# Performance work log

Hardware: AMD Instinct MI355X
Metric: run time of the kernel (lower is better)

The kernel has to match this reference:

```python
import jax, jax.numpy as jnp
import numpy as np
import math

VOCAB, SEQ, D_MODEL, H, D_FF, N_LAYERS = 32000, 2048, 768, 12, 3072, 6
D_K = D_MODEL // H
EPS = 1e-7


def _pos_encoding(seq, d):
    pos = jnp.arange(seq, dtype=jnp.float32)[:, None]
    i = jnp.arange(d)[None, :]
    rates = 1.0 / jnp.power(10000.0, (2 * (i // 2)).astype(jnp.float32) / d)
    ang = pos * rates
    return jnp.where(i % 2 == 0, jnp.sin(ang), jnp.cos(ang))  # [seq, d]


def _layernorm(x, alpha, beta):
    # faithful to source: scalar alpha/beta, population std, std+eps in denom
    mean = jnp.mean(x, axis=-1, keepdims=True)
    std = jnp.std(x, axis=-1, keepdims=True)
    return alpha * (x - mean) / (std + EPS) + beta


def setup_inputs() -> dict:
    key = jax.random.key(0)
    ks = jax.random.split(key, 16)
    s = 0.02
    d, f, n = D_MODEL, D_FF, N_LAYERS
    inp = {
        'tokens': jax.random.randint(ks[0], (2, SEQ), 0, VOCAB),
        'emb': jax.random.normal(ks[1], (VOCAB, d), jnp.float32) * s,
        'Wq': jax.random.normal(ks[2], (n, d, d), jnp.float32) * s,
        'bq': jnp.zeros((n, d), jnp.float32),
        'Wk': jax.random.normal(ks[3], (n, d, d), jnp.float32) * s,
        'bk': jnp.zeros((n, d), jnp.float32),
        'Wv': jax.random.normal(ks[4], (n, d, d), jnp.float32) * s,
        'bv': jnp.zeros((n, d), jnp.float32),
        'Wo': jax.random.normal(ks[5], (n, d, d), jnp.float32) * s,
        'bo': jnp.zeros((n, d), jnp.float32),
        'W1': jax.random.normal(ks[6], (n, d, f), jnp.float32) * s,
        'b1': jnp.zeros((n, f), jnp.float32),
        'W2': jax.random.normal(ks[7], (n, f, d), jnp.float32) * s,
        'b2': jnp.zeros((n, d), jnp.float32),
        'ln_alpha': jnp.ones((n, 2), jnp.float32),  # source inits alpha AND beta to ones
        'ln_beta': jnp.ones((n, 2), jnp.float32),
    }
    return inp


def reference(tokens, emb, Wq, bq, Wk, bk, Wv, bv, Wo, bo, W1, b1, W2, b2, ln_alpha, ln_beta):
    B, S = tokens.shape
    x = emb[tokens] * math.sqrt(D_MODEL)          # [B,S,D]
    pe = _pos_encoding(SEQ, D_MODEL)[:S]
    x = x + (x + pe)
    for l in range(N_LAYERS):
        # --- self-attention sublayer (pre-norm then residual add) ---
        h = _layernorm(x, ln_alpha[l, 0], ln_beta[l, 0])
        q = (h @ Wq[l] + bq[l]).reshape(B, S, H, D_K)
        k = (h @ Wk[l] + bk[l]).reshape(B, S, H, D_K)
        v = (h @ Wv[l] + bv[l]).reshape(B, S, H, D_K)
        scores = jnp.einsum('bqhd,bkhd->bhqk', q, k) / math.sqrt(D_K)
        attn = jax.nn.softmax(scores, axis=-1)
        o = jnp.einsum('bhqk,bkhd->bqhd', attn, v).reshape(B, S, D_MODEL)
        x = x + (o @ Wo[l] + bo[l])
        # --- feed-forward sublayer ---
        h = _layernorm(x, ln_alpha[l, 1], ln_beta[l, 1])
        ff = jax.nn.relu(h @ W1[l] + b1[l]) @ W2[l] + b2[l]
        x = x + ff
    return x
```

## Files before the change

kernel.cpp:

```cpp
#include <hip/hip_runtime.h>
#include <cstdint>

#define SEQ 2048
#define DM 768
#define NH 12
#define DKH 64
#define DFF 3072
#define NL 6
#define NTOK 4096
#define SM_SCALE 0.18033688f

typedef __attribute__((ext_vector_type(8))) short bf16x8;
typedef __attribute__((ext_vector_type(4))) float f32x4;

static __device__ __forceinline__ unsigned short f2b(float f) {
    unsigned int u = __builtin_bit_cast(unsigned int, f);
    unsigned int lsb = (u >> 16) & 1;
    u += 0x7fffu + lsb;
    return (unsigned short)(u >> 16);
}

static __device__ __forceinline__ unsigned int cvtpk2(float a, float b) {
    unsigned int r;
    asm("v_cvt_pk_bf16_f32 %0, %1, %2" : "=v"(r) : "v"(a), "v"(b));
    return r;
}

__global__ __launch_bounds__(256) void embed_k(const int* __restrict__ tokens,
                                               const float* __restrict__ emb,
                                               float* __restrict__ x)
{
    int srow = blockIdx.y;
    int d = blockIdx.x * 256 + threadIdx.x;
    int s = srow & (SEQ - 1);
    int tok = tokens[srow];
    float val = 2.0f * 27.712812921102035f * emb[(size_t)tok * DM + d];
    int half2 = (d >> 1) * 2;
    float freq = expf(-(float)half2 * (9.210340371976184f / (float)DM));
    float ang = (float)s * freq;
    val += (d & 1) ? cosf(ang) : sinf(ang);
    x[(size_t)srow * DM + d] = val;
}

__global__ __launch_bounds__(256) void ln_k(const float* __restrict__ x,
                                            unsigned short* __restrict__ h,
                                            const float* __restrict__ alpha_p,
                                            const float* __restrict__ beta_p)
{
    int lane = threadIdx.x & 63;
    int wv = threadIdx.x >> 6;
    int row = blockIdx.x * 4 + wv;
    const float* xr = x + (size_t)row * DM;
    float4 v0 = *(const float4*)&xr[lane * 4];
    float4 v1 = *(const float4*)&xr[256 + lane * 4];
    float4 v2 = *(const float4*)&xr[512 + lane * 4];
    float s  = v0.x + v0.y + v0.z + v0.w + v1.x + v1.y + v1.z + v1.w
             + v2.x + v2.y + v2.z + v2.w;
    float sq = v0.x*v0.x + v0.y*v0.y + v0.z*v0.z + v0.w*v0.w
             + v1.x*v1.x + v1.y*v1.y + v1.z*v1.z + v1.w*v1.w
             + v2.x*v2.x + v2.y*v2.y + v2.z*v2.z + v2.w*v2.w;
#pragma unroll
    for (int m = 1; m < 64; m <<= 1) {
        s  += __shfl_xor(s, m);
        sq += __shfl_xor(sq, m);
    }
    float mean = s * (1.0f / DM);
    float var  = sq * (1.0f / DM) - mean * mean;
    float stdv = sqrtf(fmaxf(var, 0.0f));
    float scale = (*alpha_p) / (stdv + 1e-7f);
    float beta  = *beta_p;
    unsigned short* hr = h + (size_t)row * DM;
    ushort4 o;
    o.x = f2b((v0.x - mean) * scale + beta); o.y = f2b((v0.y - mean) * scale + beta);
    o.z = f2b((v0.z - mean) * scale + beta); o.w = f2b((v0.w - mean) * scale + beta);
    *(ushort4*)&hr[lane * 4] = o;
    o.x = f2b((v1.x - mean) * scale + beta); o.y = f2b((v1.y - mean) * scale + beta);
    o.z = f2b((v1.z - mean) * scale + beta); o.w = f2b((v1.w - mean) * scale + beta);
    *(ushort4*)&hr[256 + lane * 4] = o;
    o.x = f2b((v2.x - mean) * scale + beta); o.y = f2b((v2.y - mean) * scale + beta);
    o.z = f2b((v2.z - mean) * scale + beta); o.w = f2b((v2.w - mean) * scale + beta);
    *(ushort4*)&hr[512 + lane * 4] = o;
}

struct WCAll { const float* src[6]; unsigned short* dst[6]; };
__global__ __launch_bounds__(256) void wconv_all_k(WCAll p)
{
    int t = blockIdx.x;
    const float* W; unsigned short* Wt; int K, N, bn, bk;
    if (t < 2304) {
        int mat = t / 576, rem = t % 576;
        W = p.src[mat]; Wt = p.dst[mat]; K = 768; N = 768;
        bn = (rem % 24) * 32; bk = (rem / 24) * 32;
    } else if (t < 4608) {
        int rem = t - 2304;
        W = p.src[4]; Wt = p.dst[4]; K = 768; N = 3072;
        bn = (rem % 96) * 32; bk = (rem / 96) * 32;
    } else {
        int rem = t - 4608;
        W = p.src[5]; Wt = p.dst[5]; K = 3072; N = 768;
        bn = (rem % 24) * 32; bk = (rem / 24) * 32;
    }
    __shared__ float tt[32][33];
    int tx = threadIdx.x & 31, ty = threadIdx.x >> 5;
#pragma unroll
    for (int i = 0; i < 4; ++i)
        tt[ty * 4 + i][tx] = W[(size_t)(bk + ty * 4 + i) * N + bn + tx];
    __syncthreads();
    int n_l = threadIdx.x >> 3;
    int k_l = (threadIdx.x & 7) * 4;
    ushort4 o;
    o.x = f2b(tt[k_l + 0][n_l]); o.y = f2b(tt[k_l + 1][n_l]);
    o.z = f2b(tt[k_l + 2][n_l]); o.w = f2b(tt[k_l + 3][n_l]);
    *(ushort4*)&Wt[(size_t)(bn + n_l) * K + bk + k_l] = o;
}

template<int OUT_MODE>
__device__ __forceinline__ void gemm_mfma_body(
    const unsigned short* __restrict__ A,
    const unsigned short* __restrict__ Bt,
    const float* __restrict__ bias,
    void* __restrict__ Cv,
    int N, int K, int kbeg, int kend, int bm, int bn)
{
    __shared__ unsigned short As[128][64];
    __shared__ unsigned short Bs[128][64];
    const int tid = threadIdx.x;
    const int lane = tid & 63;
    const int w = tid >> 6;
    const int wm = (w >> 1) << 6;
    const int wn = (w & 1) << 6;
    const int rgrp = lane >> 3;
    const int chunk = (lane & 7) ^ rgrp;
    const size_t a_src = (size_t)(bm + w * 32 + rgrp) * K + chunk * 8;
    const size_t b_src = (size_t)(bn + w * 32 + rgrp) * K + chunk * 8;

    f32x4 acc[4][4] = {};

    for (int kt = kbeg; kt < kend; kt += 64) {
        __syncthreads();
#pragma unroll
        for (int i = 0; i < 4; ++i) {
            __builtin_amdgcn_global_load_lds(
                (const __attribute__((address_space(1))) void*)(A + a_src + (size_t)(i * 8) * K + kt),
                (__attribute__((address_space(3))) void*)&As[w * 32 + i * 8][0], 16, 0, 0);
            __builtin_amdgcn_global_load_lds(
                (const __attribute__((address_space(1))) void*)(Bt + b_src + (size_t)(i * 8) * K + kt),
                (__attribute__((address_space(3))) void*)&Bs[w * 32 + i * 8][0], 16, 0, 0);
        }
        __syncthreads();
#pragma unroll
        for (int kk = 0; kk < 2; ++kk) {
            bf16x8 af[4], bfr[4];
            const int kb = kk * 64 + ((lane >> 4) << 4);
#pragma unroll
            for (int i = 0; i < 4; ++i) {
                int m = wm + i * 16 + (lane & 15);
                af[i] = *(const bf16x8*)((const char*)&As[0][0] + m * 128 + (kb ^ ((m & 7) << 4)));
                int n = wn + i * 16 + (lane & 15);
                bfr[i] = *(const bf16x8*)((const char*)&Bs[0][0] + n * 128 + (kb ^ ((n & 7) << 4)));
            }
            __builtin_amdgcn_s_setprio(1);
#pragma unroll
            for (int i = 0; i < 4; ++i)
#pragma unroll
                for (int j = 0; j < 4; ++j)
                    acc[i][j] = __builtin_amdgcn_mfma_f32_16x16x32_bf16(af[i], bfr[j], acc[i][j], 0, 0, 0);
            __builtin_amdgcn_s_setprio(0);
        }
    }
    const int cl = lane & 15, rg = lane >> 4;
#pragma unroll
    for (int i = 0; i < 4; ++i) {
        int row0 = bm + wm + i * 16 + rg * 4;
#pragma unroll
        for (int j = 0; j < 4; ++j) {
            int col = bn + wn + j * 16 + cl;
            float bv = (OUT_MODE == 5 && kbeg > 0) ? 0.0f : bias[col];
            if (OUT_MODE == 4) {
                int bb = row0 >> 11;
                int s  = row0 & 2047;
                int hh = col >> 6, d = col & 63;
                ushort4 o;
                o.x = f2b(acc[i][j][0] + bv); o.y = f2b(acc[i][j][1] + bv);
                o.z = f2b(acc[i][j][2] + bv); o.w = f2b(acc[i][j][3] + bv);
                *(ushort4*)&((unsigned short*)Cv)[(((size_t)(bb * 12 + hh) * 64 + d) << 11) + s] = o;
            } else {
#pragma unroll
                for (int r = 0; r < 4; ++r) {
                    float val = acc[i][j][r] + bv;
                    size_t idx = (size_t)(row0 + r) * N + col;
                    if (OUT_MODE == 2) {
                        ((unsigned short*)Cv)[idx] = f2b(fmaxf(val, 0.0f));
                    } else if (OUT_MODE == 3) {
                        ((unsigned short*)Cv)[idx] = f2b(val);
                    } else if (OUT_MODE == 6) {
                        ((unsigned short*)Cv)[idx] = f2b(val * SM_SCALE);
                    } else if (OUT_MODE == 5) {
                        atomicAdd(&((float*)Cv)[idx], val);
                    } else {
                        ((float*)Cv)[idx] += val;
                    }
                }
            }
        }
    }
}

static __device__ __forceinline__ void xcd_swz(int gx, int& bm, int& bn)
{
    int flat = blockIdx.y * gx + blockIdx.x;
    int nwg = gx * gridDim.y;
    int wg = (flat & 7) * (nwg >> 3) + (flat >> 3);
    bm = (wg / gx) * 128;
    bn = (wg % gx) * 128;
}

template<int OUT_MODE>
__global__ __launch_bounds__(256) void gemm_b(const unsigned short* __restrict__ A,
                                              const unsigned short* __restrict__ Bt,
                                              const float* __restrict__ bias,
                                              void* __restrict__ C, int N, int K)
{
    int bm, bn; xcd_swz(gridDim.x, bm, bn);
    gemm_mfma_body<OUT_MODE>(A, Bt, bias, C, N, K, 0, K, bm, bn);
}

__global__ __launch_bounds__(256) void gemm_sk(const unsigned short* __restrict__ A,
                                               const unsigned short* __restrict__ Bt,
                                               const float* __restrict__ bias,
                                               float* __restrict__ C, int N, int K)
{
    int bm, bn; xcd_swz(gridDim.x, bm, bn);
    int half = K >> 1;
    gemm_mfma_body<5>(A, Bt, bias, C, N, K, blockIdx.z * half, blockIdx.z * half + half,
                      bm, bn);
}

struct QKVArgsB {
    const unsigned short *wq, *wk, *wv;
    const float *bq, *bk, *bv;
    unsigned short *q, *k, *vt;
};
__global__ __launch_bounds__(256) void gemm_qkv_b(const unsigned short* __restrict__ h, QKVArgsB p)
{
    int bm, bn; xcd_swz(gridDim.x, bm, bn);
    if (blockIdx.z == 0)
        gemm_mfma_body<6>(h, p.wq, p.bq, p.q, DM, DM, 0, DM, bm, bn);
    else if (blockIdx.z == 1)
        gemm_mfma_body<3>(h, p.wk, p.bk, p.k, DM, DM, 0, DM, bm, bn);
    else
        gemm_mfma_body<4>(h, p.wv, p.bv, p.vt, DM, DM, 0, DM, bm, bn);
}

__global__ __launch_bounds__(256) void attn_m(const unsigned short* __restrict__ qg,
                                              const unsigned short* __restrict__ kg,
                                              const unsigned short* __restrict__ vt,
                                              unsigned short* __restrict__ og)
{
    __shared__ unsigned short Ks[2][64 * 64];
    __shared__ unsigned short Vs[2][64 * 64];
    __shared__ unsigned short Ps[4 * 16 * 64];
    const int tid = threadIdx.x;
    const int lane = tid & 63;
    const int w = tid >> 6;
    const int cl = lane & 15, g = lane >> 4;
    const int flat = blockIdx.x;
    const int r8 = flat >> 3;
    const int qt = r8 & 31;
    const int hb = ((r8 >> 5) << 3) + (flat & 7);
    const int b = hb >= 12;
    const int h = hb - b * 12;
    const int qrow0 = (b << 11) + qt * 64;
    const int krow0 = (b << 11);
    const int srow8 = lane >> 3;
    const int c8 = (lane & 7) ^ srow8;
    const int swz = (cl & 7) << 4;

    bf16x8 qf[2];
#pragma unroll
    for (int sl = 0; sl < 2; ++sl)
        qf[sl] = *(const bf16x8*)(qg + (size_t)(qrow0 + w * 16 + cl) * DM
                                  + h * 64 + sl * 32 + g * 8);

    bf16x8 ones;
#pragma unroll
    for (int j = 0; j < 8; ++j) ones[j] = (short)0x3F80;

    f32x4 oa[4] = {};
    f32x4 la = {};

    const unsigned short* ksrc = kg + (size_t)(krow0 + w * 16 + srow8) * DM + h * 64 + c8 * 8;
    const unsigned short* vsrc = vt + ((size_t)((b * 12 + h) * 64) + w * 16 + srow8) * SEQ + c8 * 8;
    char* pbase = (char*)Ps + w * 2048;

#define STAGE(kt_, c_)                                                                         \
    {                                                                                          \
        _Pragma("unroll")                                                                      \
        for (int t = 0; t < 2; ++t) {                                                          \
            __builtin_amdgcn_global_load_lds(                                                  \
                (const __attribute__((address_space(1))) void*)(ksrc + (size_t)((kt_) * 64 + t * 8) * DM), \
                (__attribute__((address_space(3))) void*)&Ks[c_][(w * 16 + t * 8) * 64], 16, 0, 0);        \
            __builtin_amdgcn_global_load_lds(                                                  \
                (const __attribute__((address_space(1))) void*)(vsrc + (size_t)(t * 8) * SEQ + (kt_) * 64), \
                (__attribute__((address_space(3))) void*)&Vs[c_][(w * 16 + t * 8) * 64], 16, 0, 0);        \
        }                                                                                      \
    }

    STAGE(0, 0);
    __syncthreads();

    for (int kt = 0; kt < SEQ / 64; ++kt) {
        const int c = kt & 1;
        if (kt + 1 < SEQ / 64)
            STAGE(kt + 1, c ^ 1);

        f32x4 st[4] = {};
#pragma unroll
        for (int sl = 0; sl < 2; ++sl) {
            bf16x8 kf[4];
#pragma unroll
            for (int ni = 0; ni < 4; ++ni) {
                int row = ni * 16 + cl;
                kf[ni] = *(const bf16x8*)((const char*)&Ks[c][0] + row * 128
                                          + ((sl * 64 + g * 16) ^ ((row & 7) << 4)));
            }
            __builtin_amdgcn_s_setprio(1);
#pragma unroll
            for (int ni = 0; ni < 4; ++ni)
                st[ni] = __builtin_amdgcn_mfma_f32_16x16x32_bf16(kf[ni], qf[sl], st[ni], 0, 0, 0);
            __builtin_amdgcn_s_setprio(0);
        }

#pragma unroll
        for (int ni = 0; ni < 4; ++ni) {
            float p0 = exp2f(st[ni][0]);
            float p1 = exp2f(st[ni][1]);
            float p2 = exp2f(st[ni][2]);
            float p3 = exp2f(st[ni][3]);
            uint2 o2;
            o2.x = cvtpk2(p0, p1);
            o2.y = cvtpk2(p2, p3);
            *(uint2*)(pbase + cl * 128 + ((ni * 32 + g * 8) ^ swz)) = o2;
        }
        asm volatile("" ::: "memory");

#pragma unroll
        for (int ks = 0; ks < 2; ++ks) {
            bf16x8 pa, vb[4];
            pa = *(const bf16x8*)(pbase + cl * 128 + ((ks * 64 + g * 16) ^ swz));
#pragma unroll
            for (int nj = 0; nj < 4; ++nj) {
                int row = nj * 16 + cl;
                vb[nj] = *(const bf16x8*)((const char*)&Vs[c][0] + row * 128
                                          + ((ks * 64 + g * 16) ^ ((row & 7) << 4)));
            }
            __builtin_amdgcn_s_setprio(1);
#pragma unroll
            for (int nj = 0; nj < 4; ++nj)
                oa[nj] = __builtin_amdgcn_mfma_f32_16x16x32_bf16(pa, vb[nj], oa[nj], 0, 0, 0);
            la = __builtin_amdgcn_mfma_f32_16x16x32_bf16(pa, ones, la, 0, 0, 0);
            __builtin_amdgcn_s_setprio(0);
        }

        __syncthreads();
    }
#undef STAGE

#pragma unroll
    for (int r = 0; r < 4; ++r) {
        float linv = 1.0f / la[r];
        int row = qrow0 + w * 16 + g * 4 + r;
#pragma unroll
        for (int nj = 0; nj < 4; ++nj)
            og[(size_t)row * DM + h * 64 + nj * 16 + cl] = f2b(oa[nj][r] * linv);
    }
}

extern "C" void kernel_launch(void* const* d_in, const int* in_sizes, int n_in,
                              void* d_out, int out_size, void* d_ws, size_t ws_size,
                              hipStream_t stream)
{
    const int*   tokens = (const int*)d_in[0];
    const float* emb    = (const float*)d_in[1];
    const float* Wq     = (const float*)d_in[2];
    const float* bq     = (const float*)d_in[3];
    const float* Wk     = (const float*)d_in[4];
    const float* bk     = (const float*)d_in[5];
    const float* Wv     = (const float*)d_in[6];
    const float* bv     = (const float*)d_in[7];
    const float* Wo     = (const float*)d_in[8];
    const float* bo     = (const float*)d_in[9];
    const float* W1     = (const float*)d_in[10];
    const float* b1     = (const float*)d_in[11];
    const float* W2     = (const float*)d_in[12];
    const float* b2     = (const float*)d_in[13];
    const float* ln_a   = (const float*)d_in[14];
    const float* ln_b   = (const float*)d_in[15];

    float* x = (float*)d_out;
    unsigned short* wq_b = (unsigned short*)d_ws;
    unsigned short* wk_b = wq_b + 589824;
    unsigned short* wv_b = wk_b + 589824;
    unsigned short* wo_b = wv_b + 589824;
    unsigned short* w1_b = wo_b + 589824;
    unsigned short* w2_b = w1_b + 2359296;
    unsigned short* h_b  = w2_b + 2359296;
    unsigned short* ob_b = h_b + 3145728;
    unsigned short* ff_b = ob_b + 3145728;
    unsigned short* q_bf = ff_b + 12582912;
    unsigned short* k_bf = q_bf + 3145728;
    unsigned short* vt_b = k_bf + 3145728;

    embed_k<<<dim3(DM / 256, NTOK), 256, 0, stream>>>(tokens, emb, x);

    for (int l = 0; l < NL; ++l) {
        const size_t wsq = (size_t)l * DM * DM;
        const size_t wsf = (size_t)l * DM * DFF;

        WCAll wc;
        wc.src[0] = Wq + wsq; wc.src[1] = Wk + wsq; wc.src[2] = Wv + wsq;
        wc.src[3] = Wo + wsq; wc.src[4] = W1 + wsf; wc.src[5] = W2 + wsf;
        wc.dst[0] = wq_b; wc.dst[1] = wk_b; wc.dst[2] = wv_b;
        wc.dst[3] = wo_b; wc.dst[4] = w1_b; wc.dst[5] = w2_b;
        wconv_all_k<<<6912, 256, 0, stream>>>(wc);

        ln_k<<<NTOK / 4, 256, 0, stream>>>(x, h_b, ln_a + l * 2 + 0, ln_b + l * 2 + 0);

        QKVArgsB p { wq_b, wk_b, wv_b, bq + l * DM, bk + l * DM, bv + l * DM,
                     q_bf, k_bf, vt_b };
        gemm_qkv_b<<<dim3(DM / 128, NTOK / 128, 3), 256, 0, stream>>>(h_b, p);

        attn_m<<<768, 256, 0, stream>>>(q_bf, k_bf, vt_b, ob_b);

        gemm_sk<<<dim3(DM / 128, NTOK / 128, 2), 256, 0, stream>>>(
            ob_b, wo_b, bo + l * DM, x, DM, DM);

        ln_k<<<NTOK / 4, 256, 0, stream>>>(x, h_b, ln_a + l * 2 + 1, ln_b + l * 2 + 1);

        gemm_b<2><<<dim3(DFF / 128, NTOK / 128), 256, 0, stream>>>(
            h_b, w1_b, b1 + l * DFF, ff_b, DFF, DM);

        gemm_sk<<<dim3(DM / 128, NTOK / 128, 2), 256, 0, stream>>>(
            ff_b, w2_b, b2 + l * DM, x, DM, DFF);
    }
}
```

Measured before the change: 1.285 ms.

## Split attention over two KV halves with a separate merge kernel

```diff
diff --git a/kernel.cpp b/kernel.cpp
--- a/kernel.cpp
+++ b/kernel.cpp
@@ -255,19 +255,23 @@
 __global__ __launch_bounds__(256) void attn_m(const unsigned short* __restrict__ qg,
                                               const unsigned short* __restrict__ kg,
                                               const unsigned short* __restrict__ vt,
-                                              unsigned short* __restrict__ og)
-{
-    __shared__ unsigned short Ks[2][64 * 64];
-    __shared__ unsigned short Vs[2][64 * 64];
+                                              float* __restrict__ opart,
+                                              float* __restrict__ lpart)
+{
+    __shared__ unsigned short Ks[64 * 64];
+    __shared__ unsigned short Vs[64 * 64];
     __shared__ unsigned short Ps[4 * 16 * 64];
     const int tid = threadIdx.x;
     const int lane = tid & 63;
     const int w = tid >> 6;
     const int cl = lane & 15, g = lane >> 4;
     const int flat = blockIdx.x;
-    const int r8 = flat >> 3;
-    const int qt = r8 & 31;
-    const int hb = ((r8 >> 5) << 3) + (flat & 7);
+    const int xcd = flat & 7;
+    const int rest = flat >> 3;
+    const int part = rest & 1;
+    const int r2 = rest >> 1;
+    const int qt = r2 & 31;
+    const int hb = (r2 >> 5) * 8 + xcd;
     const int b = hb >= 12;
     const int h = hb - b * 12;
     const int qrow0 = (b << 11) + qt * 64;
@@ -293,26 +297,19 @@
     const unsigned short* vsrc = vt + ((size_t)((b * 12 + h) * 64) + w * 16 + srow8) * SEQ + c8 * 8;
     char* pbase = (char*)Ps + w * 2048;
 
-#define STAGE(kt_, c_)                                                                         \
-    {                                                                                          \
-        _Pragma("unroll")                                                                      \
-        for (int t = 0; t < 2; ++t) {                                                          \
-            __builtin_amdgcn_global_load_lds(                                                  \
-                (const __attribute__((address_space(1))) void*)(ksrc + (size_t)((kt_) * 64 + t * 8) * DM), \
-                (__attribute__((address_space(3))) void*)&Ks[c_][(w * 16 + t * 8) * 64], 16, 0, 0);        \
-            __builtin_amdgcn_global_load_lds(                                                  \
-                (const __attribute__((address_space(1))) void*)(vsrc + (size_t)(t * 8) * SEQ + (kt_) * 64), \
-                (__attribute__((address_space(3))) void*)&Vs[c_][(w * 16 + t * 8) * 64], 16, 0, 0);        \
-        }                                                                                      \
-    }
-
-    STAGE(0, 0);
-    __syncthreads();
-
-    for (int kt = 0; kt < SEQ / 64; ++kt) {
-        const int c = kt & 1;
-        if (kt + 1 < SEQ / 64)
-            STAGE(kt + 1, c ^ 1);
+    const int kt0 = part * 16;
+    for (int kt = kt0; kt < kt0 + 16; ++kt) {
+        __syncthreads();
+#pragma unroll
+        for (int t = 0; t < 2; ++t) {
+            __builtin_amdgcn_global_load_lds(
+                (const __attribute__((address_space(1))) void*)(ksrc + (size_t)(kt * 64 + t * 8) * DM),
+                (__attribute__((address_space(3))) void*)&Ks[(w * 16 + t * 8) * 64], 16, 0, 0);
+            __builtin_amdgcn_global_load_lds(
+                (const __attribute__((address_space(1))) void*)(vsrc + (size_t)(t * 8) * SEQ + kt * 64),
+                (__attribute__((address_space(3))) void*)&Vs[(w * 16 + t * 8) * 64], 16, 0, 0);
+        }
+        __syncthreads();
 
         f32x4 st[4] = {};
 #pragma unroll
@@ -321,7 +318,7 @@
 #pragma unroll
             for (int ni = 0; ni < 4; ++ni) {
                 int row = ni * 16 + cl;
-                kf[ni] = *(const bf16x8*)((const char*)&Ks[c][0] + row * 128
+                kf[ni] = *(const bf16x8*)((const char*)Ks + row * 128
                                           + ((sl * 64 + g * 16) ^ ((row & 7) << 4)));
             }
             __builtin_amdgcn_s_setprio(1);
@@ -351,7 +348,7 @@
 #pragma unroll
             for (int nj = 0; nj < 4; ++nj) {
                 int row = nj * 16 + cl;
-                vb[nj] = *(const bf16x8*)((const char*)&Vs[c][0] + row * 128
+                vb[nj] = *(const bf16x8*)((const char*)Vs + row * 128
                                           + ((ks * 64 + g * 16) ^ ((row & 7) << 4)));
             }
             __builtin_amdgcn_s_setprio(1);
@@ -361,19 +358,42 @@
             la = __builtin_amdgcn_mfma_f32_16x16x32_bf16(pa, ones, la, 0, 0, 0);
             __builtin_amdgcn_s_setprio(0);
         }
-
-        __syncthreads();
-    }
-#undef STAGE
-
+    }
+
+    float* op = opart + (size_t)part * NTOK * DM;
 #pragma unroll
     for (int r = 0; r < 4; ++r) {
-        float linv = 1.0f / la[r];
         int row = qrow0 + w * 16 + g * 4 + r;
 #pragma unroll
         for (int nj = 0; nj < 4; ++nj)
-            og[(size_t)row * DM + h * 64 + nj * 16 + cl] = f2b(oa[nj][r] * linv);
-    }
+            op[(size_t)row * DM + h * 64 + nj * 16 + cl] = oa[nj][r];
+    }
+    if (cl == 0) {
+#pragma unroll
+        for (int r = 0; r < 4; ++r) {
+            int row = qrow0 + w * 16 + g * 4 + r;
+            lpart[(size_t)part * NTOK * NH + (size_t)row * NH + h] = la[r];
+        }
+    }
+}
+
+__global__ __launch_bounds__(192) void merge_k(const float* __restrict__ opart,
+                                               const float* __restrict__ lpart,
+                                               unsigned short* __restrict__ ob)
+{
+    int row = blockIdx.x;
+    int d = threadIdx.x * 4;
+    int h = d >> 6;
+    float l = lpart[(size_t)row * NH + h] + lpart[(size_t)NTOK * NH + (size_t)row * NH + h];
+    float linv = 1.0f / l;
+    float4 o0 = *(const float4*)&opart[(size_t)row * DM + d];
+    float4 o1 = *(const float4*)&opart[(size_t)NTOK * DM + (size_t)row * DM + d];
+    ushort4 o;
+    o.x = f2b((o0.x + o1.x) * linv);
+    o.y = f2b((o0.y + o1.y) * linv);
+    o.z = f2b((o0.z + o1.z) * linv);
+    o.w = f2b((o0.w + o1.w) * linv);
+    *(ushort4*)&ob[(size_t)row * DM + d] = o;
 }
 
 extern "C" void kernel_launch(void* const* d_in, const int* in_sizes, int n_in,
@@ -410,6 +430,8 @@
     unsigned short* q_bf = ff_b + 12582912;
     unsigned short* k_bf = q_bf + 3145728;
     unsigned short* vt_b = k_bf + 3145728;
+    float* opart = (float*)(vt_b + 3145728);
+    float* lpart = opart + 2 * 3145728;
 
     embed_k<<<dim3(DM / 256, NTOK), 256, 0, stream>>>(tokens, emb, x);
 
@@ -430,7 +452,8 @@
                      q_bf, k_bf, vt_b };
         gemm_qkv_b<<<dim3(DM / 128, NTOK / 128, 3), 256, 0, stream>>>(h_b, p);
 
-        attn_m<<<768, 256, 0, stream>>>(q_bf, k_bf, vt_b, ob_b);
+        attn_m<<<1536, 256, 0, stream>>>(q_bf, k_bf, vt_b, opart, lpart);
+        merge_k<<<NTOK, 192, 0, stream>>>(opart, lpart, ob_b);
 
         gemm_sk<<<dim3(DM / 128, NTOK / 128, 2), 256, 0, stream>>>(
             ob_b, wo_b, bo + l * DM, x, DM, DM);
```

Result: slower. 1.314 ms (+2.2%).
